# Optimization experiments

Hardware: AMD Instinct MI355X
Metric: run time of the kernel (lower is better)

Reference implementation:

```python
import jax, jax.numpy as jnp
import numpy as np

B, N, C, H = 4, 2048, 1024, 16
D = C // H  # head_dim = 64

def setup_inputs() -> dict:
    key = jax.random.key(0)
    k1, k2, k3, k4, k5, k6 = jax.random.split(key, 6)
    x = jax.random.normal(k1, (B, N, C), dtype=jnp.float32)
    rope_cos = jax.random.uniform(k2, (N, D), dtype=jnp.float32)
    rope_sin = jax.random.uniform(k3, (N, D), dtype=jnp.float32)
    w_qkv = jax.random.normal(k4, (3 * C, C), dtype=jnp.float32) * (C ** -0.5)
    w_proj = jax.random.normal(k5, (C, C), dtype=jnp.float32) * (C ** -0.5)
    b_proj = jax.random.normal(k6, (C,), dtype=jnp.float32) * 0.01
    return {"x": x, "rope_cos": rope_cos, "rope_sin": rope_sin,
            "w_qkv": w_qkv, "w_proj": w_proj, "b_proj": b_proj}

def _rotate_half(x):
    x1, x2 = jnp.split(x, 2, axis=-1)
    return jnp.concatenate((-x2, x1), axis=-1)

def _apply_rope(x, cos, sin):
    # x: [B,H,N,D]; cos/sin: [N,D] broadcast over B,H
    return x * cos + _rotate_half(x) * sin

def reference(x, rope_cos, rope_sin, w_qkv, w_proj, b_proj):
    Bc, Nc, Cc = x.shape
    scale = D ** -0.5
    qkv = jnp.einsum('bnc,fc->bnf', x, w_qkv)            # [B,N,3C]
    qkv = qkv.reshape(Bc, Nc, 3, H, D).transpose(2, 0, 3, 1, 4)  # [3,B,H,N,D]
    q, k, v = qkv[0], qkv[1], qkv[2]
    q = _apply_rope(q, rope_cos, rope_sin)
    k = _apply_rope(k, rope_cos, rope_sin)
    attn = jnp.einsum('bhnd,bhmd->bhnm', q, k) * scale   # [B,H,N,N]
    attn = jax.nn.softmax(attn, axis=-1)
    out = jnp.einsum('bhnm,bhmd->bhnd', attn, v)         # [B,H,N,D]
    out = out.transpose(0, 2, 1, 3).reshape(Bc, Nc, Cc)  # [B,N,C]
    return jnp.einsum('bnc,fc->bnf', out, w_proj) + b_proj
```

## Files before the change

### kernel.cpp

```cpp
#include <hip/hip_runtime.h>

#define MM   8192
#define CC   1024
#define F3   3072
#define NN   2048
#define HH   16
#define DD   64
#define QSCALE 0.1803368801111731f

typedef __attribute__((ext_vector_type(8))) __bf16 bf16x8;
typedef __attribute__((ext_vector_type(4))) float floatx4;
typedef __attribute__((ext_vector_type(4))) unsigned uintx4;

__device__ __forceinline__ unsigned short f2b(float f) {
  union { float f; unsigned int u; } v; v.f = f;
  unsigned int r = v.u + 0x7fffu + ((v.u >> 16) & 1u);
  return (unsigned short)(r >> 16);
}
__device__ __forceinline__ float b2f(unsigned short b) {
  union { unsigned int u; float f; } v; v.u = ((unsigned int)b) << 16;
  return v.f;
}

__device__ __forceinline__ void gl_lds16(const unsigned short* g, unsigned short* l) {
  __builtin_amdgcn_global_load_lds((const __attribute__((address_space(1))) void*)g,
                                   (__attribute__((address_space(3))) void*)l, 16, 0, 0);
}

__global__ __launch_bounds__(256) void f32_to_bf16_k(const float* __restrict__ in,
                                                     unsigned short* __restrict__ out, int n4) {
  int i = blockIdx.x * 256 + threadIdx.x;
  if (i < n4) {
    float4 v = ((const float4*)in)[i];
    ushort4 o;
    o.x = f2b(v.x); o.y = f2b(v.y); o.z = f2b(v.z); o.w = f2b(v.w);
    ((ushort4*)out)[i] = o;
  }
}

template <int F, bool BF16OUT, bool ROPE>
__global__ __launch_bounds__(512, 2) void gemm256(const unsigned short* __restrict__ A,
                                                  const unsigned short* __restrict__ Bm,
                                                  void* __restrict__ Cout,
                                                  const float* __restrict__ bias,
                                                  const float* __restrict__ rcp,
                                                  const float* __restrict__ spp, int K) {
  __shared__ alignas(16) unsigned short lA[2][256 * 64];
  __shared__ alignas(16) unsigned short lB[2][256 * 64];
  const int tid = threadIdx.x, lane = tid & 63, wave = tid >> 6;
  const int r16 = lane & 15, q4 = lane >> 4;
  const int wm = wave & 1, wn = wave >> 1;

  const int id = blockIdx.x;
  const int xcd = id & 7, slot = id >> 3;
  const int rx = xcd * 4 + (slot & 3), cy = slot >> 2;
  const int rowBase = rx * 256, colBase = cy * 256;

#define CHOFF(base, c) ((size_t)((base) + ((c) >> 3)) * K + ((((c) & 7) ^ (((c) >> 3) & 7)) << 3))
  size_t aoff[4], boff[4];
#pragma unroll
  for (int i = 0; i < 4; ++i) {
    aoff[i] = CHOFF(rowBase, tid + i * 512);
    boff[i] = CHOFF(colBase, tid + i * 512);
  }
#undef CHOFF

#define STAGEP(kt, bsel) do { const int _k0 = (kt) * 64; \
    gl_lds16(A + aoff[0] + _k0, &lA[bsel][(tid) * 8]); \
    gl_lds16(A + aoff[1] + _k0, &lA[bsel][(tid + 512) * 8]); \
    gl_lds16(A + aoff[2] + _k0, &lA[bsel][(tid + 1024) * 8]); \
    gl_lds16(A + aoff[3] + _k0, &lA[bsel][(tid + 1536) * 8]); \
    gl_lds16(Bm + boff[0] + _k0, &lB[bsel][(tid) * 8]); \
    gl_lds16(Bm + boff[1] + _k0, &lB[bsel][(tid + 512) * 8]); \
    gl_lds16(Bm + boff[2] + _k0, &lB[bsel][(tid + 1024) * 8]); \
    gl_lds16(Bm + boff[3] + _k0, &lB[bsel][(tid + 1536) * 8]); } while (0)

  floatx4 acc[8][4];
  const floatx4 z = {0.f, 0.f, 0.f, 0.f};
#pragma unroll
  for (int i = 0; i < 8; ++i)
#pragma unroll
    for (int j = 0; j < 4; ++j) acc[i][j] = z;

  const int nt = K / 64;

  STAGEP(0, 0);
  STAGEP(1, 1);
  asm volatile("s_waitcnt vmcnt(8)" ::: "memory");
  __builtin_amdgcn_s_barrier();
  __builtin_amdgcn_sched_barrier(0);

  for (int t = 0; t < nt; ++t) {
    const int bs = t & 1;
    const unsigned short* la = &lA[bs][0];
    const unsigned short* lb = &lB[bs][0];
    bf16x8 af[8][2];
#pragma unroll
    for (int im = 0; im < 8; ++im) {
      int row = wm * 128 + im * 16 + r16, r7 = row & 7;
      af[im][0] = *(const bf16x8*)(la + row * 64 + ((q4 ^ r7) << 3));
      af[im][1] = *(const bf16x8*)(la + row * 64 + (((4 + q4) ^ r7) << 3));
    }
#pragma unroll
    for (int jf = 0; jf < 4; ++jf) {
      int row = wn * 64 + jf * 16 + r16, r7 = row & 7;
      bf16x8 bv0 = *(const bf16x8*)(lb + row * 64 + ((q4 ^ r7) << 3));
      bf16x8 bv1 = *(const bf16x8*)(lb + row * 64 + (((4 + q4) ^ r7) << 3));
      __builtin_amdgcn_s_setprio(1);
#pragma unroll
      for (int im = 0; im < 8; ++im) {
        acc[im][jf] = __builtin_amdgcn_mfma_f32_16x16x32_bf16(af[im][0], bv0, acc[im][jf], 0, 0, 0);
        acc[im][jf] = __builtin_amdgcn_mfma_f32_16x16x32_bf16(af[im][1], bv1, acc[im][jf], 0, 0, 0);
      }
      __builtin_amdgcn_s_setprio(0);
    }

    __builtin_amdgcn_s_barrier();
    __builtin_amdgcn_sched_barrier(0);
    if (t + 2 < nt) {
      STAGEP(t + 2, bs);
      asm volatile("s_waitcnt vmcnt(8)" ::: "memory");
    } else {
      asm volatile("s_waitcnt vmcnt(0)" ::: "memory");
    }
    __builtin_amdgcn_sched_barrier(0);
    __builtin_amdgcn_s_barrier();
    __builtin_amdgcn_sched_barrier(0);
  }
#undef STAGEP

  if (ROPE) {
    int head = (colBase >> 6) + wn;
    if (head < 32) {
      const bool isq = head < 16;
#pragma unroll
      for (int im = 0; im < 8; ++im)
#pragma unroll
        for (int jf = 0; jf < 2; ++jf)
#pragma unroll
          for (int r = 0; r < 4; ++r) {
            int grow = rowBase + wm * 128 + im * 16 + q4 * 4 + r;
            int n = grow & (NN - 1);
            int dp = jf * 16 + r16;
            float x0 = acc[im][jf][r], x1 = acc[im][jf + 2][r];
            float c0 = rcp[n * DD + dp],      s0v = spp[n * DD + dp];
            float c1 = rcp[n * DD + dp + 32], s1v = spp[n * DD + dp + 32];
            float y0 = x0 * c0 - x1 * s0v;
            float y1 = x1 * c1 + x0 * s1v;
            if (isq) { y0 *= QSCALE; y1 *= QSCALE; }
            acc[im][jf][r] = y0;
            acc[im][jf + 2][r] = y1;
          }
    }
  }

#pragma unroll
  for (int im = 0; im < 8; ++im)
#pragma unroll
    for (int jf = 0; jf < 4; ++jf)
#pragma unroll
      for (int r = 0; r < 4; ++r) {
        int grow = rowBase + wm * 128 + im * 16 + q4 * 4 + r;
        int gcol = colBase + wn * 64 + jf * 16 + r16;
        if (BF16OUT)
          ((unsigned short*)Cout)[(size_t)grow * F + gcol] = f2b(acc[im][jf][r]);
        else
          ((float*)Cout)[(size_t)grow * F + gcol] = acc[im][jf][r] + bias[gcol];
      }
}

template <int F, bool BF16OUT, bool ROPE>
__global__ __launch_bounds__(512, 2) void gemm_p(const unsigned short* __restrict__ A,
                                                 const unsigned short* __restrict__ Bm,
                                                 void* __restrict__ Cout,
                                                 const float* __restrict__ bias,
                                                 const float* __restrict__ rcp,
                                                 const float* __restrict__ spp, int K) {
  __shared__ alignas(16) unsigned short lA[3][128 * 64];
  __shared__ alignas(16) unsigned short lB[3][256 * 64];
  const int tid = threadIdx.x, lane = tid & 63, wave = tid >> 6;
  const int r16 = lane & 15, q4 = lane >> 4;
  const int wm = wave & 1, wn = wave >> 1;

  const int id = blockIdx.x;
  const int xcd = id & 7, slot = id >> 3;
  const int rx = xcd * 8 + (slot & 7), cy = slot >> 3;
  const int rowBase = rx * 128, colBase = cy * 256;

  const int cA0 = tid, cA1 = tid + 512;
  const int cB0 = tid, cB1 = tid + 512, cB2 = tid + 1024, cB3 = tid + 1536;
#define CHOFF(base, c) ((size_t)((base) + ((c) >> 3)) * K + ((((c) & 7) ^ (((c) >> 3) & 7)) << 3))
  const size_t aoff0 = CHOFF(rowBase, cA0), aoff1 = CHOFF(rowBase, cA1);
  const size_t boff0 = CHOFF(colBase, cB0), boff1 = CHOFF(colBase, cB1);
  const size_t boff2 = CHOFF(colBase, cB2), boff3 = CHOFF(colBase, cB3);
#undef CHOFF

#define STAGEP(kt, bsel) do { const int _k0 = (kt) * 64; \
    gl_lds16(A + aoff0 + _k0, &lA[bsel][cA0 * 8]); \
    gl_lds16(A + aoff1 + _k0, &lA[bsel][cA1 * 8]); \
    gl_lds16(Bm + boff0 + _k0, &lB[bsel][cB0 * 8]); \
    gl_lds16(Bm + boff1 + _k0, &lB[bsel][cB1 * 8]); \
    gl_lds16(Bm + boff2 + _k0, &lB[bsel][cB2 * 8]); \
    gl_lds16(Bm + boff3 + _k0, &lB[bsel][cB3 * 8]); } while (0)

  floatx4 acc[4][4];
  const floatx4 z = {0.f, 0.f, 0.f, 0.f};
#pragma unroll
  for (int i = 0; i < 4; ++i)
#pragma unroll
    for (int j = 0; j < 4; ++j) acc[i][j] = z;

  const int nt = K / 64;

  STAGEP(0, 0);
  STAGEP(1, 1);
  STAGEP(2, 2);
  asm volatile("s_waitcnt vmcnt(12)" ::: "memory");
  __builtin_amdgcn_s_barrier();
  __builtin_amdgcn_sched_barrier(0);

  int bs = 0;
  for (int t = 0; t < nt; ++t) {
    const unsigned short* la = &lA[bs][0];
    const unsigned short* lb = &lB[bs][0];
    bf16x8 af[4][2], bv[4][2];
#pragma unroll
    for (int im = 0; im < 4; ++im) {
      int row = wm * 64 + im * 16 + r16, r7 = row & 7;
      af[im][0] = *(const bf16x8*)(la + row * 64 + ((q4 ^ r7) << 3));
      af[im][1] = *(const bf16x8*)(la + row * 64 + (((4 + q4) ^ r7) << 3));
    }
#pragma unroll
    for (int jf = 0; jf < 4; ++jf) {
      int row = wn * 64 + jf * 16 + r16, r7 = row & 7;
      bv[jf][0] = *(const bf16x8*)(lb + row * 64 + ((q4 ^ r7) << 3));
      bv[jf][1] = *(const bf16x8*)(lb + row * 64 + (((4 + q4) ^ r7) << 3));
    }
    __builtin_amdgcn_s_setprio(1);
#pragma unroll
    for (int jf = 0; jf < 4; ++jf)
#pragma unroll
      for (int im = 0; im < 4; ++im) {
        acc[im][jf] = __builtin_amdgcn_mfma_f32_16x16x32_bf16(af[im][0], bv[jf][0], acc[im][jf], 0, 0, 0);
        acc[im][jf] = __builtin_amdgcn_mfma_f32_16x16x32_bf16(af[im][1], bv[jf][1], acc[im][jf], 0, 0, 0);
      }
    __builtin_amdgcn_s_setprio(0);

    __builtin_amdgcn_s_barrier();
    __builtin_amdgcn_sched_barrier(0);
    if (t + 3 < nt) {
      STAGEP(t + 3, bs);
      asm volatile("s_waitcnt vmcnt(12)" ::: "memory");
    } else {
      asm volatile("s_waitcnt vmcnt(0)" ::: "memory");
    }
    __builtin_amdgcn_sched_barrier(0);
    __builtin_amdgcn_s_barrier();
    __builtin_amdgcn_sched_barrier(0);
    bs = (bs == 2) ? 0 : bs + 1;
  }
#undef STAGEP

  if (ROPE) {
    int head = (colBase >> 6) + wn;
    if (head < 32) {
      const bool isq = head < 16;
#pragma unroll
      for (int im = 0; im < 4; ++im)
#pragma unroll
        for (int jf = 0; jf < 2; ++jf)
#pragma unroll
          for (int r = 0; r < 4; ++r) {
            int grow = rowBase + wm * 64 + im * 16 + q4 * 4 + r;
            int n = grow & (NN - 1);
            int dp = jf * 16 + r16;
            float x0 = acc[im][jf][r], x1 = acc[im][jf + 2][r];
            float c0 = rcp[n * DD + dp],      s0v = spp[n * DD + dp];
            float c1 = rcp[n * DD + dp + 32], s1v = spp[n * DD + dp + 32];
            float y0 = x0 * c0 - x1 * s0v;
            float y1 = x1 * c1 + x0 * s1v;
            if (isq) { y0 *= QSCALE; y1 *= QSCALE; }
            acc[im][jf][r] = y0;
            acc[im][jf + 2][r] = y1;
          }
    }
  }

#pragma unroll
  for (int im = 0; im < 4; ++im)
#pragma unroll
    for (int jf = 0; jf < 4; ++jf)
#pragma unroll
      for (int r = 0; r < 4; ++r) {
        int grow = rowBase + wm * 64 + im * 16 + q4 * 4 + r;
        int gcol = colBase + wn * 64 + jf * 16 + r16;
        if (BF16OUT)
          ((unsigned short*)Cout)[(size_t)grow * F + gcol] = f2b(acc[im][jf][r]);
        else
          ((float*)Cout)[(size_t)grow * F + gcol] = acc[im][jf][r] + bias[gcol];
      }
}

__global__ __launch_bounds__(256, 4) void attn_k(const unsigned short* __restrict__ qkv,
                                                 unsigned short* __restrict__ obuf) {
  __shared__ alignas(16) unsigned short sK[64 * 64];
  __shared__ alignas(16) unsigned short sVT[64 * 64];

  const int tid = threadIdx.x, lane = tid & 63, wave = tid >> 6;
  const int r16 = lane & 15, q4 = lane >> 4;

  const int id = blockIdx.x + (int)gridDim.x * blockIdx.y;
  const int xcd = id & 7, slot = id >> 3;
  const int bh = xcd * 8 + (slot >> 4);
  const int q0 = (slot & 15) * 128;
  const int b = bh >> 4, h = bh & 15;
  const unsigned short* qbase = qkv + (size_t)(b * NN) * F3 + h * DD;

  bf16x8 qf[2][2];
#pragma unroll
  for (int im = 0; im < 2; ++im)
#pragma unroll
    for (int kk = 0; kk < 2; ++kk)
      qf[im][kk] = *(const bf16x8*)(qbase +
          (size_t)(q0 + wave * 32 + im * 16 + r16) * F3 + kk * 32 + q4 * 8);

  const floatx4 z = {0.f, 0.f, 0.f, 0.f};
  floatx4 o[2][4];
  float lacc[2] = {0.f, 0.f};
#pragma unroll
  for (int im = 0; im < 2; ++im)
    for (int jd = 0; jd < 4; ++jd) o[im][jd] = z;

  const int krow0 = tid >> 3, kc8 = tid & 7;
  const int vkvp = tid >> 3, vc8 = tid & 7;
  const int mp = (vkvp & 16) | ((vkvp & 4) << 1) | ((vkvp & 2) << 1) |
                 ((vkvp & 8) >> 2) | (vkvp & 1);

  const unsigned short* kvb = qbase;
  int4 kreg0 = *(const int4*)(kvb + (size_t)krow0 * F3 + CC + kc8 * 8);
  int4 kreg1 = *(const int4*)(kvb + (size_t)(krow0 + 32) * F3 + CC + kc8 * 8);
  int4 vreg0 = *(const int4*)(kvb + (size_t)(2 * vkvp) * F3 + 2 * CC + vc8 * 8);
  int4 vreg1 = *(const int4*)(kvb + (size_t)(2 * vkvp + 1) * F3 + 2 * CC + vc8 * 8);

  for (int t = 0; t < NN / 64; ++t) {
    __syncthreads();

    *(int4*)(&sK[krow0 * 64 + ((kc8 ^ (krow0 & 7)) << 3)]) = kreg0;
    *(int4*)(&sK[(krow0 + 32) * 64 + ((kc8 ^ ((krow0 + 32) & 7)) << 3)]) = kreg1;
    {
      const unsigned* a0 = (const unsigned*)&vreg0;
      const unsigned* a1 = (const unsigned*)&vreg1;
#pragma unroll
      for (int w = 0; w < 4; ++w) {
        unsigned lo = __builtin_amdgcn_perm(a1[w], a0[w], 0x05040100u);
        unsigned hi = __builtin_amdgcn_perm(a1[w], a0[w], 0x07060302u);
        int d0 = vc8 * 8 + 2 * w;
        int sw0 = (2 * w + vc8) & 7;
        int sw1 = (2 * w + 1 + vc8) & 7;
        *(unsigned*)(&sVT[d0 * 64 + (((mp >> 2) ^ sw0) << 3) + 2 * (mp & 3)]) = lo;
        *(unsigned*)(&sVT[(d0 + 1) * 64 + (((mp >> 2) ^ sw1) << 3) + 2 * (mp & 3)]) = hi;
      }
    }

    if (t + 1 < NN / 64) {
      const unsigned short* nb = qkv + (size_t)(b * NN + (t + 1) * 64) * F3 + h * DD;
      kreg0 = *(const int4*)(nb + (size_t)krow0 * F3 + CC + kc8 * 8);
      kreg1 = *(const int4*)(nb + (size_t)(krow0 + 32) * F3 + CC + kc8 * 8);
      vreg0 = *(const int4*)(nb + (size_t)(2 * vkvp) * F3 + 2 * CC + vc8 * 8);
      vreg1 = *(const int4*)(nb + (size_t)(2 * vkvp + 1) * F3 + 2 * CC + vc8 * 8);
    }

    __syncthreads();

    floatx4 s[2][4];
    __builtin_amdgcn_s_setprio(1);
#pragma unroll
    for (int jn = 0; jn < 4; ++jn) {
      int row = jn * 16 + r16;
      bf16x8 kf0 = *(const bf16x8*)(&sK[row * 64 + ((q4 ^ (row & 7)) << 3)]);
      bf16x8 kf1 = *(const bf16x8*)(&sK[row * 64 + (((4 + q4) ^ (row & 7)) << 3)]);
#pragma unroll
      for (int im = 0; im < 2; ++im) {
        floatx4 a = z;
        a = __builtin_amdgcn_mfma_f32_16x16x32_bf16(kf0, qf[im][0], a, 0, 0, 0);
        a = __builtin_amdgcn_mfma_f32_16x16x32_bf16(kf1, qf[im][1], a, 0, 0, 0);
        s[im][jn] = a;
      }
    }
    __builtin_amdgcn_s_setprio(0);

    bf16x8 pf[2][2];
#pragma unroll
    for (int im = 0; im < 2; ++im) {
#pragma unroll
      for (int kk = 0; kk < 2; ++kk) {
        uintx4 pk;
#pragma unroll
        for (int j2 = 0; j2 < 2; ++j2) {
          int jn = 2 * kk + j2;
          float p0 = __builtin_amdgcn_exp2f(s[im][jn][0]);
          float p1 = __builtin_amdgcn_exp2f(s[im][jn][1]);
          float p2 = __builtin_amdgcn_exp2f(s[im][jn][2]);
          float p3 = __builtin_amdgcn_exp2f(s[im][jn][3]);
          lacc[im] += (p0 + p1) + (p2 + p3);
          asm("v_cvt_pk_bf16_f32 %0, %1, %2" : "=v"(pk[2 * j2]) : "v"(p0), "v"(p1));
          asm("v_cvt_pk_bf16_f32 %0, %1, %2" : "=v"(pk[2 * j2 + 1]) : "v"(p2), "v"(p3));
        }
        pf[im][kk] = __builtin_bit_cast(bf16x8, pk);
      }
    }

    __builtin_amdgcn_s_setprio(1);
#pragma unroll
    for (int jd = 0; jd < 4; ++jd) {
      int d = jd * 16 + r16;
      int swr = (d + (d >> 3)) & 7;
      bf16x8 vf0 = *(const bf16x8*)(&sVT[d * 64 + ((q4 ^ swr) << 3)]);
      bf16x8 vf1 = *(const bf16x8*)(&sVT[d * 64 + (((4 + q4) ^ swr) << 3)]);
#pragma unroll
      for (int im = 0; im < 2; ++im) {
        o[im][jd] = __builtin_amdgcn_mfma_f32_16x16x32_bf16(pf[im][0], vf0, o[im][jd], 0, 0, 0);
        o[im][jd] = __builtin_amdgcn_mfma_f32_16x16x32_bf16(pf[im][1], vf1, o[im][jd], 0, 0, 0);
      }
    }
    __builtin_amdgcn_s_setprio(0);
  }

#pragma unroll
  for (int im = 0; im < 2; ++im) {
    float l = lacc[im];
    l += __shfl_xor(l, 16);
    l += __shfl_xor(l, 32);
    float inv = 1.0f / l;
#pragma unroll
    for (int r = 0; r < 4; ++r) {
      float invr = __shfl(inv, q4 * 4 + r);
      int row = q0 + wave * 32 + im * 16 + q4 * 4 + r;
#pragma unroll
      for (int jd = 0; jd < 4; ++jd) {
        int col = h * DD + jd * 16 + r16;
        obuf[(size_t)(b * NN + row) * CC + col] = f2b(o[im][jd][r] * invr);
      }
    }
  }
}

extern "C" void kernel_launch(void* const* d_in, const int* in_sizes, int n_in,
                              void* d_out, int out_size, void* d_ws, size_t ws_size,
                              hipStream_t stream) {
  const float* x     = (const float*)d_in[0];
  const float* rc    = (const float*)d_in[1];
  const float* rs    = (const float*)d_in[2];
  const float* wqkv  = (const float*)d_in[3];
  const float* wproj = (const float*)d_in[4];
  const float* bproj = (const float*)d_in[5];
  float* out = (float*)d_out;

  char* w = (char*)d_ws;
  unsigned short* xb     = (unsigned short*)(w);
  unsigned short* wqkvb  = (unsigned short*)(w + 16777216);
  unsigned short* wprojb = (unsigned short*)(w + 23068672);
  unsigned short* qkvb   = (unsigned short*)(w + 25165824);
  unsigned short* obuf   = (unsigned short*)(w + 75497472);

  f32_to_bf16_k<<<(MM * CC / 4 + 255) / 256, 256, 0, stream>>>(x, xb, MM * CC / 4);
  f32_to_bf16_k<<<(F3 * CC / 4 + 255) / 256, 256, 0, stream>>>(wqkv, wqkvb, F3 * CC / 4);
  f32_to_bf16_k<<<(CC * CC / 4 + 255) / 256, 256, 0, stream>>>(wproj, wprojb, CC * CC / 4);

  gemm256<F3, true, true><<<384, 512, 0, stream>>>(
      xb, wqkvb, qkvb, nullptr, rc, rs, CC);

  attn_k<<<dim3(NN / 128, 4 * HH), 256, 0, stream>>>(qkvb, obuf);

  gemm_p<CC, false, false><<<256, 512, 0, stream>>>(
      obuf, wprojb, out, bproj, nullptr, nullptr, CC);
}
```

Baseline: 281.7 us.

## Restructure QKV GEMM main loop into quarter phases and double attention query tile

The QKV GEMM loop now issues the next tile's global-to-LDS loads at the top of each iteration and splits the MFMA work into four barrier-separated quarters. Each quarter loads only half of the A or B fragments, which lowers register pressure and interleaves LDS reads with MFMA across waves. The attention kernel now processes 256 query rows per block (64 per wave) instead of 128, so each K/V tile staged in LDS is reused by twice as many queries. It launches half as many blocks with a 1-D grid and a lower occupancy hint. The risks are more barriers per GEMM iteration, higher register use and lower occupancy in attention, and fewer blocks to spread across CUs.

```diff
diff --git a/kernel.cpp b/kernel.cpp
--- a/kernel.cpp
+++ b/kernel.cpp
@@ -39,12 +39,12 @@
 }
 
 template <int F, bool BF16OUT, bool ROPE>
-__global__ __launch_bounds__(512, 2) void gemm256(const unsigned short* __restrict__ A,
-                                                  const unsigned short* __restrict__ Bm,
-                                                  void* __restrict__ Cout,
-                                                  const float* __restrict__ bias,
-                                                  const float* __restrict__ rcp,
-                                                  const float* __restrict__ spp, int K) {
+__global__ __launch_bounds__(512, 2) void gemm256v2(const unsigned short* __restrict__ A,
+                                                    const unsigned short* __restrict__ Bm,
+                                                    void* __restrict__ Cout,
+                                                    const float* __restrict__ bias,
+                                                    const float* __restrict__ rcp,
+                                                    const float* __restrict__ spp, int K) {
   __shared__ alignas(16) unsigned short lA[2][256 * 64];
   __shared__ alignas(16) unsigned short lB[2][256 * 64];
   const int tid = threadIdx.x, lane = tid & 63, wave = tid >> 6;
@@ -85,45 +85,87 @@
   const int nt = K / 64;
 
   STAGEP(0, 0);
-  STAGEP(1, 1);
-  asm volatile("s_waitcnt vmcnt(8)" ::: "memory");
+  asm volatile("s_waitcnt vmcnt(0)" ::: "memory");
   __builtin_amdgcn_s_barrier();
   __builtin_amdgcn_sched_barrier(0);
 
   for (int t = 0; t < nt; ++t) {
-    const int bs = t & 1;
-    const unsigned short* la = &lA[bs][0];
-    const unsigned short* lb = &lB[bs][0];
-    bf16x8 af[8][2];
-#pragma unroll
-    for (int im = 0; im < 8; ++im) {
+    const int p = t & 1;
+    const unsigned short* la = &lA[p][0];
+    const unsigned short* lb = &lB[p][0];
+
+    if (t + 1 < nt) STAGEP(t + 1, p ^ 1);
+    bf16x8 af[4][2], bv[4][2];
+#pragma unroll
+    for (int im = 0; im < 4; ++im) {
       int row = wm * 128 + im * 16 + r16, r7 = row & 7;
       af[im][0] = *(const bf16x8*)(la + row * 64 + ((q4 ^ r7) << 3));
       af[im][1] = *(const bf16x8*)(la + row * 64 + (((4 + q4) ^ r7) << 3));
     }
 #pragma unroll
-    for (int jf = 0; jf < 4; ++jf) {
+    for (int jf = 0; jf < 2; ++jf) {
       int row = wn * 64 + jf * 16 + r16, r7 = row & 7;
-      bf16x8 bv0 = *(const bf16x8*)(lb + row * 64 + ((q4 ^ r7) << 3));
-      bf16x8 bv1 = *(const bf16x8*)(lb + row * 64 + (((4 + q4) ^ r7) << 3));
-      __builtin_amdgcn_s_setprio(1);
-#pragma unroll
-      for (int im = 0; im < 8; ++im) {
-        acc[im][jf] = __builtin_amdgcn_mfma_f32_16x16x32_bf16(af[im][0], bv0, acc[im][jf], 0, 0, 0);
-        acc[im][jf] = __builtin_amdgcn_mfma_f32_16x16x32_bf16(af[im][1], bv1, acc[im][jf], 0, 0, 0);
-      }
-      __builtin_amdgcn_s_setprio(0);
-    }
-
-    __builtin_amdgcn_s_barrier();
-    __builtin_amdgcn_sched_barrier(0);
-    if (t + 2 < nt) {
-      STAGEP(t + 2, bs);
-      asm volatile("s_waitcnt vmcnt(8)" ::: "memory");
-    } else {
-      asm volatile("s_waitcnt vmcnt(0)" ::: "memory");
-    }
-    __builtin_amdgcn_sched_barrier(0);
+      bv[jf][0] = *(const bf16x8*)(lb + row * 64 + ((q4 ^ r7) << 3));
+      bv[jf][1] = *(const bf16x8*)(lb + row * 64 + (((4 + q4) ^ r7) << 3));
+    }
+    __builtin_amdgcn_s_barrier();
+    __builtin_amdgcn_s_setprio(1);
+#pragma unroll
+    for (int jf = 0; jf < 2; ++jf)
+#pragma unroll
+      for (int im = 0; im < 4; ++im) {
+        acc[im][jf] = __builtin_amdgcn_mfma_f32_16x16x32_bf16(af[im][0], bv[jf][0], acc[im][jf], 0, 0, 0);
+        acc[im][jf] = __builtin_amdgcn_mfma_f32_16x16x32_bf16(af[im][1], bv[jf][1], acc[im][jf], 0, 0, 0);
+      }
+    __builtin_amdgcn_s_setprio(0);
+    __builtin_amdgcn_s_barrier();
+
+#pragma unroll
+    for (int jf = 2; jf < 4; ++jf) {
+      int row = wn * 64 + jf * 16 + r16, r7 = row & 7;
+      bv[jf][0] = *(const bf16x8*)(lb + row * 64 + ((q4 ^ r7) << 3));
+      bv[jf][1] = *(const bf16x8*)(lb + row * 64 + (((4 + q4) ^ r7) << 3));
+    }
+    __builtin_amdgcn_s_barrier();
+    __builtin_amdgcn_s_setprio(1);
+#pragma unroll
+    for (int jf = 2; jf < 4; ++jf)
+#pragma unroll
+      for (int im = 0; im < 4; ++im) {
+        acc[im][jf] = __builtin_amdgcn_mfma_f32_16x16x32_bf16(af[im][0], bv[jf][0], acc[im][jf], 0, 0, 0);
+        acc[im][jf] = __builtin_amdgcn_mfma_f32_16x16x32_bf16(af[im][1], bv[jf][1], acc[im][jf], 0, 0, 0);
+      }
+    __builtin_amdgcn_s_setprio(0);
+    __builtin_amdgcn_s_barrier();
+
+#pragma unroll
+    for (int im = 0; im < 4; ++im) {
+      int row = wm * 128 + (im + 4) * 16 + r16, r7 = row & 7;
+      af[im][0] = *(const bf16x8*)(la + row * 64 + ((q4 ^ r7) << 3));
+      af[im][1] = *(const bf16x8*)(la + row * 64 + (((4 + q4) ^ r7) << 3));
+    }
+    __builtin_amdgcn_s_barrier();
+    __builtin_amdgcn_s_setprio(1);
+#pragma unroll
+    for (int jf = 0; jf < 2; ++jf)
+#pragma unroll
+      for (int im = 0; im < 4; ++im) {
+        acc[im + 4][jf] = __builtin_amdgcn_mfma_f32_16x16x32_bf16(af[im][0], bv[jf][0], acc[im + 4][jf], 0, 0, 0);
+        acc[im + 4][jf] = __builtin_amdgcn_mfma_f32_16x16x32_bf16(af[im][1], bv[jf][1], acc[im + 4][jf], 0, 0, 0);
+      }
+    __builtin_amdgcn_s_setprio(0);
+    __builtin_amdgcn_s_barrier();
+
+    __builtin_amdgcn_s_setprio(1);
+#pragma unroll
+    for (int jf = 2; jf < 4; ++jf)
+#pragma unroll
+      for (int im = 0; im < 4; ++im) {
+        acc[im + 4][jf] = __builtin_amdgcn_mfma_f32_16x16x32_bf16(af[im][0], bv[jf][0], acc[im + 4][jf], 0, 0, 0);
+        acc[im + 4][jf] = __builtin_amdgcn_mfma_f32_16x16x32_bf16(af[im][1], bv[jf][1], acc[im + 4][jf], 0, 0, 0);
+      }
+    __builtin_amdgcn_s_setprio(0);
+    asm volatile("s_waitcnt vmcnt(0)" ::: "memory");
     __builtin_amdgcn_s_barrier();
     __builtin_amdgcn_sched_barrier(0);
   }
@@ -301,7 +343,7 @@
       }
 }
 
-__global__ __launch_bounds__(256, 4) void attn_k(const unsigned short* __restrict__ qkv,
+__global__ __launch_bounds__(256, 2) void attn_k(const unsigned short* __restrict__ qkv,
                                                  unsigned short* __restrict__ obuf) {
   __shared__ alignas(16) unsigned short sK[64 * 64];
   __shared__ alignas(16) unsigned short sVT[64 * 64];
@@ -309,26 +351,26 @@
   const int tid = threadIdx.x, lane = tid & 63, wave = tid >> 6;
   const int r16 = lane & 15, q4 = lane >> 4;
 
-  const int id = blockIdx.x + (int)gridDim.x * blockIdx.y;
+  const int id = blockIdx.x;
   const int xcd = id & 7, slot = id >> 3;
-  const int bh = xcd * 8 + (slot >> 4);
-  const int q0 = (slot & 15) * 128;
+  const int bh = xcd * 8 + (slot >> 3);
+  const int q0 = (slot & 7) * 256;
   const int b = bh >> 4, h = bh & 15;
   const unsigned short* qbase = qkv + (size_t)(b * NN) * F3 + h * DD;
 
-  bf16x8 qf[2][2];
-#pragma unroll
-  for (int im = 0; im < 2; ++im)
+  bf16x8 qf[4][2];
+#pragma unroll
+  for (int im = 0; im < 4; ++im)
 #pragma unroll
     for (int kk = 0; kk < 2; ++kk)
       qf[im][kk] = *(const bf16x8*)(qbase +
-          (size_t)(q0 + wave * 32 + im * 16 + r16) * F3 + kk * 32 + q4 * 8);
+          (size_t)(q0 + wave * 64 + im * 16 + r16) * F3 + kk * 32 + q4 * 8);
 
   const floatx4 z = {0.f, 0.f, 0.f, 0.f};
-  floatx4 o[2][4];
-  float lacc[2] = {0.f, 0.f};
-#pragma unroll
-  for (int im = 0; im < 2; ++im)
+  floatx4 o[4][4];
+  float lacc[4] = {0.f, 0.f, 0.f, 0.f};
+#pragma unroll
+  for (int im = 0; im < 4; ++im)
     for (int jd = 0; jd < 4; ++jd) o[im][jd] = z;
 
   const int krow0 = tid >> 3, kc8 = tid & 7;
@@ -372,7 +414,7 @@
 
     __syncthreads();
 
-    floatx4 s[2][4];
+    floatx4 s[4][4];
     __builtin_amdgcn_s_setprio(1);
 #pragma unroll
     for (int jn = 0; jn < 4; ++jn) {
@@ -380,7 +422,7 @@
       bf16x8 kf0 = *(const bf16x8*)(&sK[row * 64 + ((q4 ^ (row & 7)) << 3)]);
       bf16x8 kf1 = *(const bf16x8*)(&sK[row * 64 + (((4 + q4) ^ (row & 7)) << 3)]);
 #pragma unroll
-      for (int im = 0; im < 2; ++im) {
+      for (int im = 0; im < 4; ++im) {
         floatx4 a = z;
         a = __builtin_amdgcn_mfma_f32_16x16x32_bf16(kf0, qf[im][0], a, 0, 0, 0);
         a = __builtin_amdgcn_mfma_f32_16x16x32_bf16(kf1, qf[im][1], a, 0, 0, 0);
@@ -389,9 +431,9 @@
     }
     __builtin_amdgcn_s_setprio(0);
 
-    bf16x8 pf[2][2];
-#pragma unroll
-    for (int im = 0; im < 2; ++im) {
+    bf16x8 pf[4][2];
+#pragma unroll
+    for (int im = 0; im < 4; ++im) {
 #pragma unroll
       for (int kk = 0; kk < 2; ++kk) {
         uintx4 pk;
@@ -418,7 +460,7 @@
       bf16x8 vf0 = *(const bf16x8*)(&sVT[d * 64 + ((q4 ^ swr) << 3)]);
       bf16x8 vf1 = *(const bf16x8*)(&sVT[d * 64 + (((4 + q4) ^ swr) << 3)]);
 #pragma unroll
-      for (int im = 0; im < 2; ++im) {
+      for (int im = 0; im < 4; ++im) {
         o[im][jd] = __builtin_amdgcn_mfma_f32_16x16x32_bf16(pf[im][0], vf0, o[im][jd], 0, 0, 0);
         o[im][jd] = __builtin_amdgcn_mfma_f32_16x16x32_bf16(pf[im][1], vf1, o[im][jd], 0, 0, 0);
       }
@@ -427,7 +469,7 @@
   }
 
 #pragma unroll
-  for (int im = 0; im < 2; ++im) {
+  for (int im = 0; im < 4; ++im) {
     float l = lacc[im];
     l += __shfl_xor(l, 16);
     l += __shfl_xor(l, 32);
@@ -435,7 +477,7 @@
 #pragma unroll
     for (int r = 0; r < 4; ++r) {
       float invr = __shfl(inv, q4 * 4 + r);
-      int row = q0 + wave * 32 + im * 16 + q4 * 4 + r;
+      int row = q0 + wave * 64 + im * 16 + q4 * 4 + r;
 #pragma unroll
       for (int jd = 0; jd < 4; ++jd) {
         int col = h * DD + jd * 16 + r16;
@@ -467,10 +509,10 @@
   f32_to_bf16_k<<<(F3 * CC / 4 + 255) / 256, 256, 0, stream>>>(wqkv, wqkvb, F3 * CC / 4);
   f32_to_bf16_k<<<(CC * CC / 4 + 255) / 256, 256, 0, stream>>>(wproj, wprojb, CC * CC / 4);
 
-  gemm256<F3, true, true><<<384, 512, 0, stream>>>(
+  gemm256v2<F3, true, true><<<384, 512, 0, stream>>>(
       xb, wqkvb, qkvb, nullptr, rc, rs, CC);
 
-  attn_k<<<dim3(NN / 128, 4 * HH), 256, 0, stream>>>(qkvb, obuf);
+  attn_k<<<512, 256, 0, stream>>>(qkvb, obuf);
 
   gemm_p<CC, false, false><<<256, 512, 0, stream>>>(
       obuf, wprojb, out, bproj, nullptr, nullptr, CC);
```

Result: no change. 279.0 us (-1.0%).
